# Performance work log

Hardware: AMD Instinct MI355X
Metric: run time of the kernel (lower is better)

Reference implementation:

```python
import jax, jax.numpy as jnp
import numpy as np

BLOCKSIZE = 128
NUM_EXPERTS = 16
TOP_K = 6
HIDDEN = 2048
INTER = 1408
TOKENS = 4096
N_BLK_H = HIDDEN // BLOCKSIZE   # 16
N_BLK_I = -(-INTER // BLOCKSIZE)  # 11 (ceil)


def setup_inputs() -> dict:
    key = jax.random.key(0)
    ks = jax.random.split(key, 8)
    x = jax.random.normal(ks[0], (TOKENS, HIDDEN), dtype=jnp.float32)
    selected_experts = jax.random.randint(ks[1], (TOKENS, TOP_K), 0, NUM_EXPERTS)
    # quantized-style weights + per-block scales (dequant = w * repeat(s, blocksize))
    w0 = jax.random.normal(ks[2], (NUM_EXPERTS, INTER, HIDDEN), dtype=jnp.float32) * 0.02
    s0 = jax.random.uniform(ks[3], (NUM_EXPERTS, INTER, N_BLK_H), dtype=jnp.float32, minval=0.5, maxval=1.5)
    w1 = jax.random.normal(ks[4], (NUM_EXPERTS, INTER, HIDDEN), dtype=jnp.float32) * 0.02
    s1 = jax.random.uniform(ks[5], (NUM_EXPERTS, INTER, N_BLK_H), dtype=jnp.float32, minval=0.5, maxval=1.5)
    w2 = jax.random.normal(ks[6], (NUM_EXPERTS, HIDDEN, INTER), dtype=jnp.float32) * 0.02
    s2 = jax.random.uniform(ks[7], (NUM_EXPERTS, HIDDEN, N_BLK_I), dtype=jnp.float32, minval=0.5, maxval=1.5)
    return {"x": x, "selected_experts": selected_experts,
            "w0": w0, "s0": s0, "w1": w1, "s1": s1, "w2": w2, "s2": s2}


def _dequant(w, s):
    # w: [E, O, I], s: [E, O, ceil(I/bs)] -> broadcast each scale over its block
    s_full = jnp.repeat(s, BLOCKSIZE, axis=-1)[..., : w.shape[-1]]
    return w * s_full


def reference(x, selected_experts, w0, s0, w1, s1, w2, s2):
    # Dequantize block-quantized expert weights.
    W0 = _dequant(w0, s0)  # gate proj [E, I, H]
    W1 = _dequant(w1, s1)  # up proj   [E, I, H]
    W2 = _dequant(w2, s2)  # down proj [E, H, I]
    # Original loops token x slot, calling expert(x[i]). Equivalent batched form:
    # compute every expert on every token, then gather by (token, slot) index.
    gate = jnp.einsum('th,eih->eti', x, W0)            # [E, T, I]
    up = jnp.einsum('th,eih->eti', x, W1)              # [E, T, I]
    act = jax.nn.silu(gate) * up                       # [E, T, I]
    all_out = jnp.einsum('eti,ehi->eth', act, W2)      # [E, T, H]
    tok = jnp.arange(x.shape[0])[:, None]              # [T, 1]
    out = all_out[selected_experts, tok]               # [T, K, H]
    return out
```

## Files before the change

### kernel.cpp

```cpp
#include <hip/hip_runtime.h>
#include <stdint.h>

#define TOKENS 4096
#define HIDDEN 2048
#define INTER  1408
#define NEXP   16
#define TOPK   6
#define NPAIR  (TOKENS*TOPK)
#define BM     128
#define MAXTILES (NPAIR/BM + NEXP)
#define MAXT2  (NPAIR/256 + NEXP)
#define NT1    (INTER/128)
#define NT2    (HIDDEN/128)

typedef __attribute__((ext_vector_type(8))) short bf16x8;
typedef __attribute__((ext_vector_type(4))) float f32x4;

__device__ __forceinline__ short f2bf(float f){
  union { float f; uint32_t u; } v; v.f = f;
  uint32_t r = (v.u + 0x7FFFu + ((v.u >> 16) & 1u)) >> 16;
  return (short)(r & 0xFFFFu);
}

__device__ __forceinline__ void gld16(const void* g, const void* l){
  __builtin_amdgcn_global_load_lds((const __attribute__((address_space(1))) void*)g,
                                   (__attribute__((address_space(3))) void*)l, 16, 0, 0);
}


__global__ void k_xcast(const float* __restrict__ x, short* __restrict__ xb){
  int i = (blockIdx.x * 256 + threadIdx.x) * 8;
  f32x4 a = *(const f32x4*)(x + i);
  f32x4 b = *(const f32x4*)(x + i + 4);
  bf16x8 o;
  #pragma unroll
  for (int j = 0; j < 4; ++j){ o[j] = f2bf(a[j]); o[4+j] = f2bf(b[j]); }
  *(bf16x8*)(xb + i) = o;
}

__global__ void k_dequant(const float* __restrict__ w, const float* __restrict__ s,
                          short* __restrict__ o, int rowlen, int nblk){
  const int row = blockIdx.x;
  const size_t base = (size_t)row * rowlen;
  for (int c = threadIdx.x * 8; c < rowlen; c += blockDim.x * 8){
    float sc = s[(size_t)row * nblk + (c >> 7)];
    f32x4 a = *(const f32x4*)(w + base + c);
    f32x4 b = *(const f32x4*)(w + base + c + 4);
    bf16x8 h;
    #pragma unroll
    for (int j = 0; j < 4; ++j){ h[j] = f2bf(a[j] * sc); h[4+j] = f2bf(b[j] * sc); }
    *(bf16x8*)(o + base + c) = h;
  }
}

__global__ void k_count(const int* __restrict__ sel, int* __restrict__ cnt){
  int p = blockIdx.x * 256 + threadIdx.x;
  if (p < NPAIR) atomicAdd(&cnt[sel[p]], 1);
}

__global__ void k_scan(const int* __restrict__ cnt, int* __restrict__ offsets,
                       int2* __restrict__ tiles, int* __restrict__ ntiles,
                       int2* __restrict__ tiles2, int* __restrict__ ntiles2){
  if (threadIdx.x != 0) return;
  int off = 0, nt = 0, nt2 = 0;
  for (int e = 0; e < NEXP; ++e){
    offsets[e] = off;
    int c = cnt[e];
    for (int m = 0; m < c; m += BM){
      int rows = c - m; if (rows > BM) rows = BM;
      tiles[nt++] = make_int2(off + m, (e << 16) | rows);
    }
    for (int m = 0; m < c; m += 256){
      int rows = c - m; if (rows > 256) rows = 256;
      tiles2[nt2++] = make_int2(off + m, (e << 16) | rows);
    }
    off += c;
  }
  offsets[NEXP] = off;
  *ntiles = nt;
  *ntiles2 = nt2;
}

__global__ void k_scatter(const int* __restrict__ sel, const int* __restrict__ offsets,
                          int* __restrict__ cursor, int* __restrict__ pair_tk){
  int p = blockIdx.x * 256 + threadIdx.x;
  if (p >= NPAIR) return;
  int e = sel[p];
  int pos = offsets[e] + atomicAdd(&cursor[e], 1);
  pair_tk[pos] = (p / TOPK) * 8 + (p % TOPK);
}


__global__ __launch_bounds__(512) void k_g1(
    const short* __restrict__ xb,
    const short* __restrict__ w0b, const short* __restrict__ w1b,
    const int2* __restrict__ tiles2, const int* __restrict__ ntiles2,
    const int* __restrict__ pair_tk, short* __restrict__ act)
{
  const int nwg = MAXT2 * NT1;
  const int orig = (int)(blockIdx.y * MAXT2 + blockIdx.x);
  const int wg = (orig & 7) * (nwg >> 3) + (orig >> 3);
  const int tx = wg % MAXT2, ty = wg / MAXT2;
  if (tx >= *ntiles2) return;
  const int2 td = tiles2[tx];
  const int mstart = td.x;
  const int e  = td.y >> 16;
  const int vr = td.y & 0xFFFF;

  __shared__ short lA[2][256 * 64];
  __shared__ short lB[2][256 * 64];

  const int tid = threadIdx.x, w = tid >> 6, lane = tid & 63;

  const short* pA[4]; const short* pB[4]; int s8[4];
  #pragma unroll
  for (int i = 0; i < 4; ++i){
    int s = w * 256 + i * 64 + lane;
    int r = s >> 3, g = (s & 7) ^ (r & 7);
    s8[i] = s * 8;
    int p = mstart + r; if (p >= NPAIR) p = NPAIR - 1;
    pA[i] = xb + (size_t)(pair_tk[p] >> 3) * HIDDEN + g * 8;
    int G = r >> 4, srow = (G >> 1) * 16 + (r & 15);
    const short* wsrc = (G & 1) ? w1b : w0b;
    pB[i] = wsrc + ((size_t)e * INTER + (size_t)ty * 128 + srow) * HIDDEN + g * 8;
  }
  auto stage = [&](short* bA, short* bB, int ko){
    #pragma unroll
    for (int i = 0; i < 4; ++i) gld16(pA[i] + ko, bA + s8[i]);
    #pragma unroll
    for (int i = 0; i < 4; ++i) gld16(pB[i] + ko, bB + s8[i]);
  };

  f32x4 acc[4][8];
  #pragma unroll
  for (int i = 0; i < 4; ++i)
    #pragma unroll
    for (int j = 0; j < 8; ++j) acc[i][j] = (f32x4)0.f;

  const int cc = lane & 15, ks = lane >> 4;
  const int sx0 = (ks ^ (cc & 7)) * 8;
  const int sx1 = ((4 | ks) ^ (cc & 7)) * 8;
  const int wm = w >> 1, wn = w & 1;
  int arow[4], brow[8];
  #pragma unroll
  for (int mf = 0; mf < 4; ++mf) arow[mf] = (wm * 64 + mf * 16 + cc) * 64;
  #pragma unroll
  for (int nf = 0; nf < 8; ++nf) brow[nf] = (wn * 128 + nf * 16 + cc) * 64;

  stage(lA[0], lB[0], 0);
  stage(lA[1], lB[1], 64);

  #pragma unroll 1
  for (int kt = 0; kt < 32; ++kt){
    const short* A = lA[kt & 1];
    const short* B = lB[kt & 1];
    if (kt < 31) asm volatile("s_waitcnt vmcnt(8)" ::: "memory");
    else         asm volatile("s_waitcnt vmcnt(0)" ::: "memory");
    __builtin_amdgcn_sched_barrier(0);
    __builtin_amdgcn_s_barrier();
    __builtin_amdgcn_sched_barrier(0);

    bf16x8 a0[4], a1[4];
    #pragma unroll
    for (int mf = 0; mf < 4; ++mf){
      a0[mf] = *(const bf16x8*)(A + arow[mf] + sx0);
      a1[mf] = *(const bf16x8*)(A + arow[mf] + sx1);
    }
    #pragma unroll
    for (int h = 0; h < 2; ++h){
      bf16x8 b0[4], b1[4];
      #pragma unroll
      for (int q = 0; q < 4; ++q){
        b0[q] = *(const bf16x8*)(B + brow[h * 4 + q] + sx0);
        b1[q] = *(const bf16x8*)(B + brow[h * 4 + q] + sx1);
      }
      #pragma unroll
      for (int q = 0; q < 4; ++q)
        #pragma unroll
        for (int mf = 0; mf < 4; ++mf)
          acc[mf][h*4+q] = __builtin_amdgcn_mfma_f32_16x16x32_bf16(a0[mf], b0[q], acc[mf][h*4+q], 0, 0, 0);
      #pragma unroll
      for (int q = 0; q < 4; ++q)
        #pragma unroll
        for (int mf = 0; mf < 4; ++mf)
          acc[mf][h*4+q] = __builtin_amdgcn_mfma_f32_16x16x32_bf16(a1[mf], b1[q], acc[mf][h*4+q], 0, 0, 0);
    }
    __builtin_amdgcn_sched_barrier(0);
    __builtin_amdgcn_s_barrier();
    __builtin_amdgcn_sched_barrier(0);
    if (kt + 2 < 32) stage(lA[kt & 1], lB[kt & 1], (kt + 2) * 64);
  }

  #pragma unroll
  for (int mf = 0; mf < 4; ++mf){
    #pragma unroll
    for (int j = 0; j < 4; ++j){
      int row = wm * 64 + mf * 16 + ks * 4 + j;
      if (row < vr){
        short* ar = act + (size_t)(mstart + row) * INTER + (size_t)ty * 128 + cc;
        #pragma unroll
        for (int q = 0; q < 4; ++q){
          float g = acc[mf][2*q][j], u = acc[mf][2*q+1][j];
          float a = g / (1.f + __expf(-g)) * u;
          ar[(wn * 4 + q) * 16] = f2bf(a);
        }
      }
    }
  }
}

__global__ __launch_bounds__(512) void k_g2(
    const short* __restrict__ act, const short* __restrict__ w2b,
    const int2* __restrict__ tiles2, const int* __restrict__ ntiles2,
    const int* __restrict__ pair_tk, float* __restrict__ out)
{
  const int nwg = MAXT2 * NT2;
  const int orig = (int)(blockIdx.y * MAXT2 + blockIdx.x);
  const int wg = (orig & 7) * (nwg >> 3) + (orig >> 3);
  const int tx = wg % MAXT2, ty = wg / MAXT2;
  if (tx >= *ntiles2) return;
  const int2 td = tiles2[tx];
  const int mstart = td.x;
  const int e  = td.y >> 16;
  const int vr = td.y & 0xFFFF;

  __shared__ short lA[2][256 * 64];
  __shared__ short lB[2][128 * 64];

  const int tid = threadIdx.x, w = tid >> 6, lane = tid & 63;

  const short* pA[4]; int s8a[4];
  #pragma unroll
  for (int i = 0; i < 4; ++i){
    int s = w * 256 + i * 64 + lane;
    int r = s >> 3, g = (s & 7) ^ (r & 7);
    s8a[i] = s * 8;
    int p = mstart + r; if (p >= NPAIR) p = NPAIR - 1;
    pA[i] = act + (size_t)p * INTER + g * 8;
  }
  const short* pB[2]; int s8b[2];
  #pragma unroll
  for (int i = 0; i < 2; ++i){
    int s = w * 128 + i * 64 + lane;
    int r = s >> 3, g = (s & 7) ^ (r & 7);
    s8b[i] = s * 8;
    pB[i] = w2b + ((size_t)e * HIDDEN + (size_t)ty * 128 + r) * INTER + g * 8;
  }
  auto stage = [&](short* bA, short* bB, int ko){
    #pragma unroll
    for (int i = 0; i < 4; ++i) gld16(pA[i] + ko, bA + s8a[i]);
    #pragma unroll
    for (int i = 0; i < 2; ++i) gld16(pB[i] + ko, bB + s8b[i]);
  };

  f32x4 acc[4][4];
  #pragma unroll
  for (int i = 0; i < 4; ++i)
    #pragma unroll
    for (int j = 0; j < 4; ++j) acc[i][j] = (f32x4)0.f;

  const int cc = lane & 15, ks = lane >> 4;
  const int sx0 = (ks ^ (cc & 7)) * 8;
  const int sx1 = ((4 | ks) ^ (cc & 7)) * 8;
  const int wm = w >> 1, wn = w & 1;
  int arow[4], brow[4];
  #pragma unroll
  for (int mf = 0; mf < 4; ++mf) arow[mf] = (wm * 64 + mf * 16 + cc) * 64;
  #pragma unroll
  for (int nf = 0; nf < 4; ++nf) brow[nf] = (wn * 64 + nf * 16 + cc) * 64;

  stage(lA[0], lB[0], 0);
  stage(lA[1], lB[1], 64);

  #pragma unroll 1
  for (int kt = 0; kt < 22; ++kt){
    const short* A = lA[kt & 1];
    const short* B = lB[kt & 1];
    if (kt < 21) asm volatile("s_waitcnt vmcnt(6)" ::: "memory");
    else         asm volatile("s_waitcnt vmcnt(0)" ::: "memory");
    __builtin_amdgcn_sched_barrier(0);
    __builtin_amdgcn_s_barrier();
    __builtin_amdgcn_sched_barrier(0);

    bf16x8 a0[4], a1[4], b0[4], b1[4];
    #pragma unroll
    for (int mf = 0; mf < 4; ++mf){
      a0[mf] = *(const bf16x8*)(A + arow[mf] + sx0);
      a1[mf] = *(const bf16x8*)(A + arow[mf] + sx1);
    }
    #pragma unroll
    for (int nf = 0; nf < 4; ++nf){
      b0[nf] = *(const bf16x8*)(B + brow[nf] + sx0);
      b1[nf] = *(const bf16x8*)(B + brow[nf] + sx1);
    }
    #pragma unroll
    for (int nf = 0; nf < 4; ++nf)
      #pragma unroll
      for (int mf = 0; mf < 4; ++mf)
        acc[mf][nf] = __builtin_amdgcn_mfma_f32_16x16x32_bf16(a0[mf], b0[nf], acc[mf][nf], 0, 0, 0);
    #pragma unroll
    for (int nf = 0; nf < 4; ++nf)
      #pragma unroll
      for (int mf = 0; mf < 4; ++mf)
        acc[mf][nf] = __builtin_amdgcn_mfma_f32_16x16x32_bf16(a1[mf], b1[nf], acc[mf][nf], 0, 0, 0);

    __builtin_amdgcn_sched_barrier(0);
    __builtin_amdgcn_s_barrier();
    __builtin_amdgcn_sched_barrier(0);
    if (kt + 2 < 22) stage(lA[kt & 1], lB[kt & 1], (kt + 2) * 64);
  }

  #pragma unroll
  for (int mf = 0; mf < 4; ++mf){
    #pragma unroll
    for (int j = 0; j < 4; ++j){
      int row = wm * 64 + mf * 16 + ks * 4 + j;
      if (row < vr){
        int ptk = pair_tk[mstart + row];
        float* orow = out + ((size_t)(ptk >> 3) * TOPK + (ptk & 7)) * HIDDEN
                      + (size_t)ty * 128 + wn * 64 + cc;
        #pragma unroll
        for (int nf = 0; nf < 4; ++nf)
          orow[nf * 16] = acc[mf][nf][j];
      }
    }
  }
}


__global__ __launch_bounds__(256) void k_gemm1(
    const short* __restrict__ xb,
    const float* __restrict__ w0, const float* __restrict__ s0,
    const float* __restrict__ w1, const float* __restrict__ s1,
    const int2* __restrict__ tiles, const int* __restrict__ ntiles,
    const int* __restrict__ pair_tk, short* __restrict__ act)
{
  if ((int)blockIdx.x >= *ntiles) return;
  const int2 td = tiles[blockIdx.x];
  const int mstart = td.x;
  const int e  = td.y >> 16;
  const int vr = td.y & 0xFFFF;
  const int tid = threadIdx.x;
  const int lane = tid & 63;

  __shared__ short lA[BM * 32];
  __shared__ short lB0[BM * 40];
  __shared__ short lB1[BM * 40];

  const int r0 = tid >> 2, r1 = 64 + (tid >> 2);
  const int seg = tid & 3;
  int p0 = mstart + r0; if (p0 >= NPAIR) p0 = NPAIR - 1;
  int p1 = mstart + r1; if (p1 >= NPAIR) p1 = NPAIR - 1;
  const short* arow0 = xb + (size_t)(pair_tk[p0] >> 3) * HIDDEN + (seg ^ ((r0 >> 1) & 3)) * 8;
  const short* arow1 = xb + (size_t)(pair_tk[p1] >> 3) * HIDDEN + (seg ^ ((r1 >> 1) & 3)) * 8;
  const short* ldsA0 = &lA[tid * 8];
  const short* ldsA1 = &lA[2048 + tid * 8];

  const int brow = tid >> 1, half = tid & 1;
  const int gbrow = blockIdx.y * BM + brow;
  const float* w0row = w0 + ((size_t)e * INTER + gbrow) * HIDDEN + half * 16;
  const float* w1row = w1 + ((size_t)e * INTER + gbrow) * HIDDEN + half * 16;
  const float* s0row = s0 + ((size_t)e * INTER + gbrow) * (HIDDEN / 128);
  const float* s1row = s1 + ((size_t)e * INTER + gbrow) * (HIDDEN / 128);
  short* lb0w = &lB0[brow * 40 + half * 16];
  short* lb1w = &lB1[brow * 40 + half * 16];

  f32x4 acc0[4][4], acc1[4][4];
  #pragma unroll
  for (int i = 0; i < 4; ++i)
    #pragma unroll
    for (int j = 0; j < 4; ++j){ acc0[i][j] = (f32x4)0.f; acc1[i][j] = (f32x4)0.f; }

  const int wm = tid >> 7, wn = (tid >> 6) & 1;
  const int cc = lane & 15, ks = lane >> 4;

  for (int kt = 0; kt < HIDDEN / 32; ++kt){
    gld16(arow0 + kt * 32, ldsA0);
    gld16(arow1 + kt * 32, ldsA1);
    {
      float sc = s0row[kt >> 2];
      const float* g = w0row + kt * 32;
      f32x4 q0 = *(const f32x4*)g,       q1 = *(const f32x4*)(g + 4),
            q2 = *(const f32x4*)(g + 8), q3 = *(const f32x4*)(g + 12);
      bf16x8 h0, h1;
      #pragma unroll
      for (int i = 0; i < 4; ++i){
        h0[i] = f2bf(q0[i] * sc); h0[4 + i] = f2bf(q1[i] * sc);
        h1[i] = f2bf(q2[i] * sc); h1[4 + i] = f2bf(q3[i] * sc);
      }
      *(bf16x8*)lb0w = h0; *(bf16x8*)(lb0w + 8) = h1;
    }
    {
      float sc = s1row[kt >> 2];
      const float* g = w1row + kt * 32;
      f32x4 q0 = *(const f32x4*)g,       q1 = *(const f32x4*)(g + 4),
            q2 = *(const f32x4*)(g + 8), q3 = *(const f32x4*)(g + 12);
      bf16x8 h0, h1;
      #pragma unroll
      for (int i = 0; i < 4; ++i){
        h0[i] = f2bf(q0[i] * sc); h0[4 + i] = f2bf(q1[i] * sc);
        h1[i] = f2bf(q2[i] * sc); h1[4 + i] = f2bf(q3[i] * sc);
      }
      *(bf16x8*)lb1w = h0; *(bf16x8*)(lb1w + 8) = h1;
    }
    __syncthreads();

    bf16x8 af[4];
    #pragma unroll
    for (int mf = 0; mf < 4; ++mf){
      int row = wm * 64 + mf * 16 + cc;
      af[mf] = *(const bf16x8*)&lA[row * 32 + ((ks ^ ((row >> 1) & 3)) * 8)];
    }
    #pragma unroll
    for (int nf = 0; nf < 4; ++nf){
      int rb = wn * 64 + nf * 16 + cc;
      bf16x8 b0 = *(const bf16x8*)&lB0[rb * 40 + ks * 8];
      bf16x8 b1 = *(const bf16x8*)&lB1[rb * 40 + ks * 8];
      #pragma unroll
      for (int mf = 0; mf < 4; ++mf)
        acc0[mf][nf] = __builtin_amdgcn_mfma_f32_16x16x32_bf16(af[mf], b0, acc0[mf][nf], 0, 0, 0);
      #pragma unroll
      for (int mf = 0; mf < 4; ++mf)
        acc1[mf][nf] = __builtin_amdgcn_mfma_f32_16x16x32_bf16(af[mf], b1, acc1[mf][nf], 0, 0, 0);
    }
    __syncthreads();
  }

  const int rbase = wm * 64 + (lane >> 4) * 4;
  #pragma unroll
  for (int mf = 0; mf < 4; ++mf){
    #pragma unroll
    for (int j = 0; j < 4; ++j){
      int row = rbase + mf * 16 + j;
      if (row < vr){
        short* ar = act + (size_t)(mstart + row) * INTER + blockIdx.y * BM + wn * 64 + cc;
        #pragma unroll
        for (int nf = 0; nf < 4; ++nf){
          float g = acc0[mf][nf][j], u = acc1[mf][nf][j];
          float a = g / (1.f + __expf(-g)) * u;
          ar[nf * 16] = f2bf(a);
        }
      }
    }
  }
}

__global__ __launch_bounds__(256) void k_gemm2(
    const short* __restrict__ act,
    const float* __restrict__ w2, const float* __restrict__ s2,
    const int2* __restrict__ tiles, const int* __restrict__ ntiles,
    const int* __restrict__ pair_tk, float* __restrict__ out)
{
  if ((int)blockIdx.x >= *ntiles) return;
  const int2 td = tiles[blockIdx.x];
  const int mstart = td.x;
  const int e  = td.y >> 16;
  const int vr = td.y & 0xFFFF;
  const int tid = threadIdx.x;
  const int lane = tid & 63;

  __shared__ short lA[BM * 32];
  __shared__ short lB[BM * 40];

  const int r0 = tid >> 2, r1 = 64 + (tid >> 2);
  const int seg = tid & 3;
  int p0 = mstart + r0; if (p0 >= NPAIR) p0 = NPAIR - 1;
  int p1 = mstart + r1; if (p1 >= NPAIR) p1 = NPAIR - 1;
  const short* arow0 = act + (size_t)p0 * INTER + (seg ^ ((r0 >> 1) & 3)) * 8;
  const short* arow1 = act + (size_t)p1 * INTER + (seg ^ ((r1 >> 1) & 3)) * 8;
  const short* ldsA0 = &lA[tid * 8];
  const short* ldsA1 = &lA[2048 + tid * 8];

  const int brow = tid >> 1, half = tid & 1;
  const int gbrow = blockIdx.y * BM + brow;
  const float* w2row = w2 + ((size_t)e * HIDDEN + gbrow) * INTER + half * 16;
  const float* s2row = s2 + ((size_t)e * HIDDEN + gbrow) * 11;
  short* lbw = &lB[brow * 40 + half * 16];

  f32x4 acc[4][4];
  #pragma unroll
  for (int i = 0; i < 4; ++i)
    #pragma unroll
    for (int j = 0; j < 4; ++j) acc[i][j] = (f32x4)0.f;

  const int wm = tid >> 7, wn = (tid >> 6) & 1;
  const int cc = lane & 15, ks = lane >> 4;

  for (int kt = 0; kt < INTER / 32; ++kt){
    gld16(arow0 + kt * 32, ldsA0);
    gld16(arow1 + kt * 32, ldsA1);
    {
      float sc = s2row[kt >> 2];
      const float* g = w2row + kt * 32;
      f32x4 q0 = *(const f32x4*)g,       q1 = *(const f32x4*)(g + 4),
            q2 = *(const f32x4*)(g + 8), q3 = *(const f32x4*)(g + 12);
      bf16x8 h0, h1;
      #pragma unroll
      for (int i = 0; i < 4; ++i){
        h0[i] = f2bf(q0[i] * sc); h0[4 + i] = f2bf(q1[i] * sc);
        h1[i] = f2bf(q2[i] * sc); h1[4 + i] = f2bf(q3[i] * sc);
      }
      *(bf16x8*)lbw = h0; *(bf16x8*)(lbw + 8) = h1;
    }
    __syncthreads();

    bf16x8 af[4];
    #pragma unroll
    for (int mf = 0; mf < 4; ++mf){
      int row = wm * 64 + mf * 16 + cc;
      af[mf] = *(const bf16x8*)&lA[row * 32 + ((ks ^ ((row >> 1) & 3)) * 8)];
    }
    #pragma unroll
    for (int nf = 0; nf < 4; ++nf){
      int rb = wn * 64 + nf * 16 + cc;
      bf16x8 b = *(const bf16x8*)&lB[rb * 40 + ks * 8];
      #pragma unroll
      for (int mf = 0; mf < 4; ++mf)
        acc[mf][nf] = __builtin_amdgcn_mfma_f32_16x16x32_bf16(af[mf], b, acc[mf][nf], 0, 0, 0);
    }
    __syncthreads();
  }

  const int rbase = wm * 64 + (lane >> 4) * 4;
  #pragma unroll
  for (int mf = 0; mf < 4; ++mf){
    #pragma unroll
    for (int j = 0; j < 4; ++j){
      int row = rbase + mf * 16 + j;
      if (row < vr){
        int ptk = pair_tk[mstart + row];
        float* orow = out + ((size_t)(ptk >> 3) * TOPK + (ptk & 7)) * HIDDEN
                      + blockIdx.y * BM + wn * 64 + cc;
        #pragma unroll
        for (int nf = 0; nf < 4; ++nf)
          orow[nf * 16] = acc[mf][nf][j];
      }
    }
  }
}


extern "C" void kernel_launch(void* const* d_in, const int* in_sizes, int n_in,
                              void* d_out, int out_size, void* d_ws, size_t ws_size,
                              hipStream_t stream)
{
  const float* x  = (const float*)d_in[0];
  const int*   sel= (const int*)  d_in[1];
  const float* w0 = (const float*)d_in[2];
  const float* s0 = (const float*)d_in[3];
  const float* w1 = (const float*)d_in[4];
  const float* s1 = (const float*)d_in[5];
  const float* w2 = (const float*)d_in[6];
  const float* s2 = (const float*)d_in[7];
  float* out = (float*)d_out;

  char* ws = (char*)d_ws;
  size_t o = 0;
  auto alloc = [&](size_t n){ size_t r = o; o = (o + n + 255) & ~(size_t)255; return r; };
  int*  cnt     = (int*) (ws + alloc(64));
  int*  cursor  = (int*) (ws + alloc(64));
  int*  offsets = (int*) (ws + alloc(68));
  int*  ntiles  = (int*) (ws + alloc(4));
  int*  ntiles2 = (int*) (ws + alloc(4));
  int2* tiles   = (int2*)(ws + alloc(MAXTILES * 8));
  int2* tiles2  = (int2*)(ws + alloc(MAXT2 * 8));
  int*  pair_tk = (int*) (ws + alloc((size_t)NPAIR * 4));
  short* xb     = (short*)(ws + alloc((size_t)TOKENS * HIDDEN * 2));
  short* act    = (short*)(ws + alloc((size_t)NPAIR * INTER * 2));
  const size_t WSZ = (size_t)NEXP * INTER * HIDDEN * 2;
  short* w0b    = (short*)(ws + alloc(WSZ));
  short* w1b    = (short*)(ws + alloc(WSZ));
  short* w2b    = (short*)(ws + alloc(WSZ));
  const bool predeq = (ws_size >= o);
  (void)in_sizes; (void)n_in; (void)out_size;

  hipMemsetAsync(ws, 0, 512, stream);

  k_xcast  <<<(TOKENS * HIDDEN) / (256 * 8), 256, 0, stream>>>(x, xb);
  k_count  <<<(NPAIR + 255) / 256, 256, 0, stream>>>(sel, cnt);
  k_scan   <<<1, 64, 0, stream>>>(cnt, offsets, tiles, ntiles, tiles2, ntiles2);
  k_scatter<<<(NPAIR + 255) / 256, 256, 0, stream>>>(sel, offsets, cursor, pair_tk);

  if (predeq){
    k_dequant<<<NEXP * INTER,  256, 0, stream>>>(w0, s0, w0b, HIDDEN, HIDDEN / 128);
    k_dequant<<<NEXP * INTER,  256, 0, stream>>>(w1, s1, w1b, HIDDEN, HIDDEN / 128);
    k_dequant<<<NEXP * HIDDEN, 256, 0, stream>>>(w2, s2, w2b, INTER, 11);
    k_g1<<<dim3(MAXT2, NT1), 512, 0, stream>>>(xb, w0b, w1b,
                                               tiles2, ntiles2, pair_tk, act);
    k_g2<<<dim3(MAXT2, NT2), 512, 0, stream>>>(act, w2b,
                                               tiles2, ntiles2, pair_tk, out);
  } else {
    k_gemm1<<<dim3(MAXTILES, NT1), 256, 0, stream>>>(xb, w0, s0, w1, s1,
                                                     tiles, ntiles, pair_tk, act);
    k_gemm2<<<dim3(MAXTILES, NT2), 256, 0, stream>>>(act, w2, s2,
                                                     tiles, ntiles, pair_tk, out);
  }
}
```

Measured before the change: 984.3 us.

## Interleave LDS reads with MFMA in sub-phases using barriers and setprio

Both grouped GEMM kernels now split each k-step into smaller sub-phases. Each sub-phase loads only the B fragments it needs from LDS, waits at a barrier, and then issues MFMAs at raised wave priority via s_setprio. This keeps waves in lockstep so the LDS reads of one wave overlap the matrix work of another, in a ping-pong style. It also moves the global prefetch and its vmcnt wait to the end of the iteration, so the wait covers the next buffer. The cost is several extra workgroup barriers per k-step, which may add synchronisation overhead.

```diff
diff --git a/kernel.cpp b/kernel.cpp
--- a/kernel.cpp
+++ b/kernel.cpp
@@ -149,46 +149,62 @@
 
   stage(lA[0], lB[0], 0);
   stage(lA[1], lB[1], 64);
+  asm volatile("s_waitcnt vmcnt(8)" ::: "memory");
+  __builtin_amdgcn_sched_barrier(0);
+  __builtin_amdgcn_s_barrier();
+  __builtin_amdgcn_sched_barrier(0);
 
   #pragma unroll 1
   for (int kt = 0; kt < 32; ++kt){
     const short* A = lA[kt & 1];
     const short* B = lB[kt & 1];
-    if (kt < 31) asm volatile("s_waitcnt vmcnt(8)" ::: "memory");
-    else         asm volatile("s_waitcnt vmcnt(0)" ::: "memory");
+    bf16x8 a0[4], a1[4];
+
+    #pragma unroll
+    for (int q = 0; q < 4; ++q){
+      if (q == 0){
+        #pragma unroll
+        for (int mf = 0; mf < 4; ++mf){
+          a0[mf] = *(const bf16x8*)(A + arow[mf] + sx0);
+          a1[mf] = *(const bf16x8*)(A + arow[mf] + sx1);
+        }
+      }
+      bf16x8 b0[2], b1[2];
+      #pragma unroll
+      for (int j = 0; j < 2; ++j){
+        b0[j] = *(const bf16x8*)(B + brow[2*q+j] + sx0);
+        b1[j] = *(const bf16x8*)(B + brow[2*q+j] + sx1);
+      }
+      __builtin_amdgcn_sched_barrier(0);
+      __builtin_amdgcn_s_barrier();
+      asm volatile("s_waitcnt lgkmcnt(0)" ::: "memory");
+      __builtin_amdgcn_sched_barrier(0);
+      __builtin_amdgcn_s_setprio(1);
+      #pragma unroll
+      for (int j = 0; j < 2; ++j)
+        #pragma unroll
+        for (int mf = 0; mf < 4; ++mf)
+          acc[mf][2*q+j] = __builtin_amdgcn_mfma_f32_16x16x32_bf16(a0[mf], b0[j], acc[mf][2*q+j], 0, 0, 0);
+      #pragma unroll
+      for (int j = 0; j < 2; ++j)
+        #pragma unroll
+        for (int mf = 0; mf < 4; ++mf)
+          acc[mf][2*q+j] = __builtin_amdgcn_mfma_f32_16x16x32_bf16(a1[mf], b1[j], acc[mf][2*q+j], 0, 0, 0);
+      __builtin_amdgcn_s_setprio(0);
+      __builtin_amdgcn_sched_barrier(0);
+      __builtin_amdgcn_s_barrier();
+      __builtin_amdgcn_sched_barrier(0);
+    }
+
+    if (kt + 2 < 32){
+      stage(lA[kt & 1], lB[kt & 1], (kt + 2) * 64);
+      asm volatile("s_waitcnt vmcnt(8)" ::: "memory");
+    } else {
+      asm volatile("s_waitcnt vmcnt(0)" ::: "memory");
+    }
     __builtin_amdgcn_sched_barrier(0);
     __builtin_amdgcn_s_barrier();
     __builtin_amdgcn_sched_barrier(0);
-
-    bf16x8 a0[4], a1[4];
-    #pragma unroll
-    for (int mf = 0; mf < 4; ++mf){
-      a0[mf] = *(const bf16x8*)(A + arow[mf] + sx0);
-      a1[mf] = *(const bf16x8*)(A + arow[mf] + sx1);
-    }
-    #pragma unroll
-    for (int h = 0; h < 2; ++h){
-      bf16x8 b0[4], b1[4];
-      #pragma unroll
-      for (int q = 0; q < 4; ++q){
-        b0[q] = *(const bf16x8*)(B + brow[h * 4 + q] + sx0);
-        b1[q] = *(const bf16x8*)(B + brow[h * 4 + q] + sx1);
-      }
-      #pragma unroll
-      for (int q = 0; q < 4; ++q)
-        #pragma unroll
-        for (int mf = 0; mf < 4; ++mf)
-          acc[mf][h*4+q] = __builtin_amdgcn_mfma_f32_16x16x32_bf16(a0[mf], b0[q], acc[mf][h*4+q], 0, 0, 0);
-      #pragma unroll
-      for (int q = 0; q < 4; ++q)
-        #pragma unroll
-        for (int mf = 0; mf < 4; ++mf)
-          acc[mf][h*4+q] = __builtin_amdgcn_mfma_f32_16x16x32_bf16(a1[mf], b1[q], acc[mf][h*4+q], 0, 0, 0);
-    }
-    __builtin_amdgcn_sched_barrier(0);
-    __builtin_amdgcn_s_barrier();
-    __builtin_amdgcn_sched_barrier(0);
-    if (kt + 2 < 32) stage(lA[kt & 1], lB[kt & 1], (kt + 2) * 64);
   }
 
   #pragma unroll
@@ -271,43 +287,62 @@
 
   stage(lA[0], lB[0], 0);
   stage(lA[1], lB[1], 64);
+  asm volatile("s_waitcnt vmcnt(6)" ::: "memory");
+  __builtin_amdgcn_sched_barrier(0);
+  __builtin_amdgcn_s_barrier();
+  __builtin_amdgcn_sched_barrier(0);
 
   #pragma unroll 1
   for (int kt = 0; kt < 22; ++kt){
     const short* A = lA[kt & 1];
     const short* B = lB[kt & 1];
-    if (kt < 21) asm volatile("s_waitcnt vmcnt(6)" ::: "memory");
-    else         asm volatile("s_waitcnt vmcnt(0)" ::: "memory");
+    bf16x8 a0[4], a1[4];
+
+    #pragma unroll
+    for (int q = 0; q < 2; ++q){
+      if (q == 0){
+        #pragma unroll
+        for (int mf = 0; mf < 4; ++mf){
+          a0[mf] = *(const bf16x8*)(A + arow[mf] + sx0);
+          a1[mf] = *(const bf16x8*)(A + arow[mf] + sx1);
+        }
+      }
+      bf16x8 b0[2], b1[2];
+      #pragma unroll
+      for (int j = 0; j < 2; ++j){
+        b0[j] = *(const bf16x8*)(B + brow[2*q+j] + sx0);
+        b1[j] = *(const bf16x8*)(B + brow[2*q+j] + sx1);
+      }
+      __builtin_amdgcn_sched_barrier(0);
+      __builtin_amdgcn_s_barrier();
+      asm volatile("s_waitcnt lgkmcnt(0)" ::: "memory");
+      __builtin_amdgcn_sched_barrier(0);
+      __builtin_amdgcn_s_setprio(1);
+      #pragma unroll
+      for (int j = 0; j < 2; ++j)
+        #pragma unroll
+        for (int mf = 0; mf < 4; ++mf)
+          acc[mf][2*q+j] = __builtin_amdgcn_mfma_f32_16x16x32_bf16(a0[mf], b0[j], acc[mf][2*q+j], 0, 0, 0);
+      #pragma unroll
+      for (int j = 0; j < 2; ++j)
+        #pragma unroll
+        for (int mf = 0; mf < 4; ++mf)
+          acc[mf][2*q+j] = __builtin_amdgcn_mfma_f32_16x16x32_bf16(a1[mf], b1[j], acc[mf][2*q+j], 0, 0, 0);
+      __builtin_amdgcn_s_setprio(0);
+      __builtin_amdgcn_sched_barrier(0);
+      __builtin_amdgcn_s_barrier();
+      __builtin_amdgcn_sched_barrier(0);
+    }
+
+    if (kt + 2 < 22){
+      stage(lA[kt & 1], lB[kt & 1], (kt + 2) * 64);
+      asm volatile("s_waitcnt vmcnt(6)" ::: "memory");
+    } else {
+      asm volatile("s_waitcnt vmcnt(0)" ::: "memory");
+    }
     __builtin_amdgcn_sched_barrier(0);
     __builtin_amdgcn_s_barrier();
     __builtin_amdgcn_sched_barrier(0);
-
-    bf16x8 a0[4], a1[4], b0[4], b1[4];
-    #pragma unroll
-    for (int mf = 0; mf < 4; ++mf){
-      a0[mf] = *(const bf16x8*)(A + arow[mf] + sx0);
-      a1[mf] = *(const bf16x8*)(A + arow[mf] + sx1);
-    }
-    #pragma unroll
-    for (int nf = 0; nf < 4; ++nf){
-      b0[nf] = *(const bf16x8*)(B + brow[nf] + sx0);
-      b1[nf] = *(const bf16x8*)(B + brow[nf] + sx1);
-    }
-    #pragma unroll
-    for (int nf = 0; nf < 4; ++nf)
-      #pragma unroll
-      for (int mf = 0; mf < 4; ++mf)
-        acc[mf][nf] = __builtin_amdgcn_mfma_f32_16x16x32_bf16(a0[mf], b0[nf], acc[mf][nf], 0, 0, 0);
-    #pragma unroll
-    for (int nf = 0; nf < 4; ++nf)
-      #pragma unroll
-      for (int mf = 0; mf < 4; ++mf)
-        acc[mf][nf] = __builtin_amdgcn_mfma_f32_16x16x32_bf16(a1[mf], b1[nf], acc[mf][nf], 0, 0, 0);
-
-    __builtin_amdgcn_sched_barrier(0);
-    __builtin_amdgcn_s_barrier();
-    __builtin_amdgcn_sched_barrier(0);
-    if (kt + 2 < 22) stage(lA[kt & 1], lB[kt & 1], (kt + 2) * 64);
   }
 
   #pragma unroll
```

Result: slower. 1.070 ms (+8.7%).

## Split K-tiles into four 32-wide LDS stages with interleaved prefetch in MoE GEMMs

Applied to the files above, without the earlier changes.

Both grouped GEMM kernels now use four LDS buffers of 32-wide K slices instead of two 64-wide ones. Each half-step issues the next global-to-LDS prefetch between its LDS reads and its MFMA block, and raises wave priority around the MFMAs. The XOR swizzle is dropped for a plain 4-chunk row layout, which may add LDS bank conflicts. The w2 dequant launch is also moved after the first GEMM; same-stream ordering is kept, so that move alone changes little.

```diff
diff --git a/kernel.cpp b/kernel.cpp
--- a/kernel.cpp
+++ b/kernel.cpp
@@ -26,6 +26,11 @@
   __builtin_amdgcn_global_load_lds((const __attribute__((address_space(1))) void*)g,
                                    (__attribute__((address_space(3))) void*)l, 16, 0, 0);
 }
+
+#define SB() __builtin_amdgcn_sched_barrier(0)
+#define BAR() __builtin_amdgcn_s_barrier()
+#define WAITV(n) asm volatile("s_waitcnt vmcnt(" #n ")" ::: "memory")
+#define WAITL() asm volatile("s_waitcnt lgkmcnt(0)" ::: "memory")
 
 
 __global__ void k_xcast(const float* __restrict__ x, short* __restrict__ xb){
@@ -107,28 +112,28 @@
   const int e  = td.y >> 16;
   const int vr = td.y & 0xFFFF;
 
-  __shared__ short lA[2][256 * 64];
-  __shared__ short lB[2][256 * 64];
+  __shared__ short lA[4][8192];
+  __shared__ short lB[4][8192];
 
   const int tid = threadIdx.x, w = tid >> 6, lane = tid & 63;
 
-  const short* pA[4]; const short* pB[4]; int s8[4];
-  #pragma unroll
-  for (int i = 0; i < 4; ++i){
-    int s = w * 256 + i * 64 + lane;
-    int r = s >> 3, g = (s & 7) ^ (r & 7);
-    s8[i] = s * 8;
+  const short* pA[2]; const short* pB[2]; int sg8[2];
+  #pragma unroll
+  for (int i = 0; i < 2; ++i){
+    int s = (w * 2 + i) * 64 + lane;
+    int r = s >> 2, j = s & 3;
+    sg8[i] = s * 8;
     int p = mstart + r; if (p >= NPAIR) p = NPAIR - 1;
-    pA[i] = xb + (size_t)(pair_tk[p] >> 3) * HIDDEN + g * 8;
+    pA[i] = xb + (size_t)(pair_tk[p] >> 3) * HIDDEN + j * 8;
     int G = r >> 4, srow = (G >> 1) * 16 + (r & 15);
     const short* wsrc = (G & 1) ? w1b : w0b;
-    pB[i] = wsrc + ((size_t)e * INTER + (size_t)ty * 128 + srow) * HIDDEN + g * 8;
-  }
-  auto stage = [&](short* bA, short* bB, int ko){
-    #pragma unroll
-    for (int i = 0; i < 4; ++i) gld16(pA[i] + ko, bA + s8[i]);
-    #pragma unroll
-    for (int i = 0; i < 4; ++i) gld16(pB[i] + ko, bB + s8[i]);
+    pB[i] = wsrc + ((size_t)e * INTER + (size_t)ty * 128 + srow) * HIDDEN + j * 8;
+  }
+  auto stage = [&](int slot, int ko){
+    #pragma unroll
+    for (int i = 0; i < 2; ++i) gld16(pA[i] + ko, &lA[slot][sg8[i]]);
+    #pragma unroll
+    for (int i = 0; i < 2; ++i) gld16(pB[i] + ko, &lB[slot][sg8[i]]);
   };
 
   f32x4 acc[4][8];
@@ -138,57 +143,59 @@
     for (int j = 0; j < 8; ++j) acc[i][j] = (f32x4)0.f;
 
   const int cc = lane & 15, ks = lane >> 4;
-  const int sx0 = (ks ^ (cc & 7)) * 8;
-  const int sx1 = ((4 | ks) ^ (cc & 7)) * 8;
+  const int kso = ks * 8;
   const int wm = w >> 1, wn = w & 1;
   int arow[4], brow[8];
   #pragma unroll
-  for (int mf = 0; mf < 4; ++mf) arow[mf] = (wm * 64 + mf * 16 + cc) * 64;
-  #pragma unroll
-  for (int nf = 0; nf < 8; ++nf) brow[nf] = (wn * 128 + nf * 16 + cc) * 64;
-
-  stage(lA[0], lB[0], 0);
-  stage(lA[1], lB[1], 64);
+  for (int mf = 0; mf < 4; ++mf) arow[mf] = (wm * 64 + mf * 16 + cc) * 32;
+  #pragma unroll
+  for (int nf = 0; nf < 8; ++nf) brow[nf] = (wn * 128 + nf * 16 + cc) * 32;
+
+  stage(0, 0); stage(1, 32); stage(2, 64); stage(3, 96);
 
   #pragma unroll 1
-  for (int kt = 0; kt < 32; ++kt){
-    const short* A = lA[kt & 1];
-    const short* B = lB[kt & 1];
-    if (kt < 31) asm volatile("s_waitcnt vmcnt(8)" ::: "memory");
-    else         asm volatile("s_waitcnt vmcnt(0)" ::: "memory");
-    __builtin_amdgcn_sched_barrier(0);
-    __builtin_amdgcn_s_barrier();
-    __builtin_amdgcn_sched_barrier(0);
-
-    bf16x8 a0[4], a1[4];
-    #pragma unroll
-    for (int mf = 0; mf < 4; ++mf){
-      a0[mf] = *(const bf16x8*)(A + arow[mf] + sx0);
-      a1[mf] = *(const bf16x8*)(A + arow[mf] + sx1);
-    }
-    #pragma unroll
-    for (int h = 0; h < 2; ++h){
-      bf16x8 b0[4], b1[4];
-      #pragma unroll
-      for (int q = 0; q < 4; ++q){
-        b0[q] = *(const bf16x8*)(B + brow[h * 4 + q] + sx0);
-        b1[q] = *(const bf16x8*)(B + brow[h * 4 + q] + sx1);
-      }
-      #pragma unroll
-      for (int q = 0; q < 4; ++q)
+  for (int t = 0; t < 32; ++t){
+    const int b = t & 1;
+    if (t == 0)      { WAITV(12); }
+    else if (t < 31) { WAITV(8);  }
+    else             { WAITV(4);  }
+    SB(); BAR(); SB();
+    {
+      bf16x8 a0[4], bb[8];
+      #pragma unroll
+      for (int mf = 0; mf < 4; ++mf) a0[mf] = *(const bf16x8*)&lA[b*2][arow[mf] + kso];
+      #pragma unroll
+      for (int nf = 0; nf < 8; ++nf) bb[nf] = *(const bf16x8*)&lB[b*2][brow[nf] + kso];
+      if (t >= 1 && t + 1 < 32) stage(((t+1)&1)*2 + 1, (t+1)*64 + 32);
+      WAITL(); SB();
+      __builtin_amdgcn_s_setprio(1);
+      #pragma unroll
+      for (int nf = 0; nf < 8; ++nf)
         #pragma unroll
         for (int mf = 0; mf < 4; ++mf)
-          acc[mf][h*4+q] = __builtin_amdgcn_mfma_f32_16x16x32_bf16(a0[mf], b0[q], acc[mf][h*4+q], 0, 0, 0);
-      #pragma unroll
-      for (int q = 0; q < 4; ++q)
+          acc[mf][nf] = __builtin_amdgcn_mfma_f32_16x16x32_bf16(a0[mf], bb[nf], acc[mf][nf], 0, 0, 0);
+      __builtin_amdgcn_s_setprio(0);
+      SB(); BAR(); SB();
+    }
+    if (t < 31) { WAITV(8); } else { WAITV(0); }
+    SB(); BAR(); SB();
+    {
+      bf16x8 a0[4], bb[8];
+      #pragma unroll
+      for (int mf = 0; mf < 4; ++mf) a0[mf] = *(const bf16x8*)&lA[b*2+1][arow[mf] + kso];
+      #pragma unroll
+      for (int nf = 0; nf < 8; ++nf) bb[nf] = *(const bf16x8*)&lB[b*2+1][brow[nf] + kso];
+      if (t + 2 < 32) stage(b*2, (t+2)*64);
+      WAITL(); SB();
+      __builtin_amdgcn_s_setprio(1);
+      #pragma unroll
+      for (int nf = 0; nf < 8; ++nf)
         #pragma unroll
         for (int mf = 0; mf < 4; ++mf)
-          acc[mf][h*4+q] = __builtin_amdgcn_mfma_f32_16x16x32_bf16(a1[mf], b1[q], acc[mf][h*4+q], 0, 0, 0);
-    }
-    __builtin_amdgcn_sched_barrier(0);
-    __builtin_amdgcn_s_barrier();
-    __builtin_amdgcn_sched_barrier(0);
-    if (kt + 2 < 32) stage(lA[kt & 1], lB[kt & 1], (kt + 2) * 64);
+          acc[mf][nf] = __builtin_amdgcn_mfma_f32_16x16x32_bf16(a0[mf], bb[nf], acc[mf][nf], 0, 0, 0);
+      __builtin_amdgcn_s_setprio(0);
+      SB(); BAR(); SB();
+    }
   }
 
   #pragma unroll
@@ -224,33 +231,31 @@
   const int e  = td.y >> 16;
   const int vr = td.y & 0xFFFF;
 
-  __shared__ short lA[2][256 * 64];
-  __shared__ short lB[2][128 * 64];
+  __shared__ short lA[4][8192];
+  __shared__ short lB[4][4096];
 
   const int tid = threadIdx.x, w = tid >> 6, lane = tid & 63;
 
-  const short* pA[4]; int s8a[4];
-  #pragma unroll
-  for (int i = 0; i < 4; ++i){
-    int s = w * 256 + i * 64 + lane;
-    int r = s >> 3, g = (s & 7) ^ (r & 7);
-    s8a[i] = s * 8;
+  const short* pA[2]; int sg8[2];
+  #pragma unroll
+  for (int i = 0; i < 2; ++i){
+    int s = (w * 2 + i) * 64 + lane;
+    int r = s >> 2, j = s & 3;
+    sg8[i] = s * 8;
     int p = mstart + r; if (p >= NPAIR) p = NPAIR - 1;
-    pA[i] = act + (size_t)p * INTER + g * 8;
-  }
-  const short* pB[2]; int s8b[2];
-  #pragma unroll
-  for (int i = 0; i < 2; ++i){
-    int s = w * 128 + i * 64 + lane;
-    int r = s >> 3, g = (s & 7) ^ (r & 7);
-    s8b[i] = s * 8;
-    pB[i] = w2b + ((size_t)e * HIDDEN + (size_t)ty * 128 + r) * INTER + g * 8;
-  }
-  auto stage = [&](short* bA, short* bB, int ko){
-    #pragma unroll
-    for (int i = 0; i < 4; ++i) gld16(pA[i] + ko, bA + s8a[i]);
-    #pragma unroll
-    for (int i = 0; i < 2; ++i) gld16(pB[i] + ko, bB + s8b[i]);
+    pA[i] = act + (size_t)p * INTER + j * 8;
+  }
+  const short* pB; int sb8;
+  {
+    int s = tid;
+    int r = s >> 2, j = s & 3;
+    sb8 = s * 8;
+    pB = w2b + ((size_t)e * HIDDEN + (size_t)ty * 128 + r) * INTER + j * 8;
+  }
+  auto stage = [&](int slot, int ko){
+    #pragma unroll
+    for (int i = 0; i < 2; ++i) gld16(pA[i] + ko, &lA[slot][sg8[i]]);
+    gld16(pB + ko, &lB[slot][sb8]);
   };
 
   f32x4 acc[4][4];
@@ -260,54 +265,59 @@
     for (int j = 0; j < 4; ++j) acc[i][j] = (f32x4)0.f;
 
   const int cc = lane & 15, ks = lane >> 4;
-  const int sx0 = (ks ^ (cc & 7)) * 8;
-  const int sx1 = ((4 | ks) ^ (cc & 7)) * 8;
+  const int kso = ks * 8;
   const int wm = w >> 1, wn = w & 1;
   int arow[4], brow[4];
   #pragma unroll
-  for (int mf = 0; mf < 4; ++mf) arow[mf] = (wm * 64 + mf * 16 + cc) * 64;
-  #pragma unroll
-  for (int nf = 0; nf < 4; ++nf) brow[nf] = (wn * 64 + nf * 16 + cc) * 64;
-
-  stage(lA[0], lB[0], 0);
-  stage(lA[1], lB[1], 64);
+  for (int mf = 0; mf < 4; ++mf) arow[mf] = (wm * 64 + mf * 16 + cc) * 32;
+  #pragma unroll
+  for (int nf = 0; nf < 4; ++nf) brow[nf] = (wn * 64 + nf * 16 + cc) * 32;
+
+  stage(0, 0); stage(1, 32); stage(2, 64); stage(3, 96);
 
   #pragma unroll 1
-  for (int kt = 0; kt < 22; ++kt){
-    const short* A = lA[kt & 1];
-    const short* B = lB[kt & 1];
-    if (kt < 21) asm volatile("s_waitcnt vmcnt(6)" ::: "memory");
-    else         asm volatile("s_waitcnt vmcnt(0)" ::: "memory");
-    __builtin_amdgcn_sched_barrier(0);
-    __builtin_amdgcn_s_barrier();
-    __builtin_amdgcn_sched_barrier(0);
-
-    bf16x8 a0[4], a1[4], b0[4], b1[4];
-    #pragma unroll
-    for (int mf = 0; mf < 4; ++mf){
-      a0[mf] = *(const bf16x8*)(A + arow[mf] + sx0);
-      a1[mf] = *(const bf16x8*)(A + arow[mf] + sx1);
-    }
-    #pragma unroll
-    for (int nf = 0; nf < 4; ++nf){
-      b0[nf] = *(const bf16x8*)(B + brow[nf] + sx0);
-      b1[nf] = *(const bf16x8*)(B + brow[nf] + sx1);
-    }
-    #pragma unroll
-    for (int nf = 0; nf < 4; ++nf)
-      #pragma unroll
-      for (int mf = 0; mf < 4; ++mf)
-        acc[mf][nf] = __builtin_amdgcn_mfma_f32_16x16x32_bf16(a0[mf], b0[nf], acc[mf][nf], 0, 0, 0);
-    #pragma unroll
-    for (int nf = 0; nf < 4; ++nf)
-      #pragma unroll
-      for (int mf = 0; mf < 4; ++mf)
-        acc[mf][nf] = __builtin_amdgcn_mfma_f32_16x16x32_bf16(a1[mf], b1[nf], acc[mf][nf], 0, 0, 0);
-
-    __builtin_amdgcn_sched_barrier(0);
-    __builtin_amdgcn_s_barrier();
-    __builtin_amdgcn_sched_barrier(0);
-    if (kt + 2 < 22) stage(lA[kt & 1], lB[kt & 1], (kt + 2) * 64);
+  for (int t = 0; t < 22; ++t){
+    const int b = t & 1;
+    if (t == 0)      { WAITV(9); }
+    else if (t < 21) { WAITV(6); }
+    else             { WAITV(3); }
+    SB(); BAR(); SB();
+    {
+      bf16x8 a0[4], bb[4];
+      #pragma unroll
+      for (int mf = 0; mf < 4; ++mf) a0[mf] = *(const bf16x8*)&lA[b*2][arow[mf] + kso];
+      #pragma unroll
+      for (int nf = 0; nf < 4; ++nf) bb[nf] = *(const bf16x8*)&lB[b*2][brow[nf] + kso];
+      if (t >= 1 && t + 1 < 22) stage(((t+1)&1)*2 + 1, (t+1)*64 + 32);
+      WAITL(); SB();
+      __builtin_amdgcn_s_setprio(1);
+      #pragma unroll
+      for (int nf = 0; nf < 4; ++nf)
+        #pragma unroll
+        for (int mf = 0; mf < 4; ++mf)
+          acc[mf][nf] = __builtin_amdgcn_mfma_f32_16x16x32_bf16(a0[mf], bb[nf], acc[mf][nf], 0, 0, 0);
+      __builtin_amdgcn_s_setprio(0);
+      SB(); BAR(); SB();
+    }
+    if (t < 21) { WAITV(6); } else { WAITV(0); }
+    SB(); BAR(); SB();
+    {
+      bf16x8 a0[4], bb[4];
+      #pragma unroll
+      for (int mf = 0; mf < 4; ++mf) a0[mf] = *(const bf16x8*)&lA[b*2+1][arow[mf] + kso];
+      #pragma unroll
+      for (int nf = 0; nf < 4; ++nf) bb[nf] = *(const bf16x8*)&lB[b*2+1][brow[nf] + kso];
+      if (t + 2 < 22) stage(b*2, (t+2)*64);
+      WAITL(); SB();
+      __builtin_amdgcn_s_setprio(1);
+      #pragma unroll
+      for (int nf = 0; nf < 4; ++nf)
+        #pragma unroll
+        for (int mf = 0; mf < 4; ++mf)
+          acc[mf][nf] = __builtin_amdgcn_mfma_f32_16x16x32_bf16(a0[mf], bb[nf], acc[mf][nf], 0, 0, 0);
+      __builtin_amdgcn_s_setprio(0);
+      SB(); BAR(); SB();
+    }
   }
 
   #pragma unroll
@@ -584,9 +594,9 @@
   if (predeq){
     k_dequant<<<NEXP * INTER,  256, 0, stream>>>(w0, s0, w0b, HIDDEN, HIDDEN / 128);
     k_dequant<<<NEXP * INTER,  256, 0, stream>>>(w1, s1, w1b, HIDDEN, HIDDEN / 128);
-    k_dequant<<<NEXP * HIDDEN, 256, 0, stream>>>(w2, s2, w2b, INTER, 11);
     k_g1<<<dim3(MAXT2, NT1), 512, 0, stream>>>(xb, w0b, w1b,
                                                tiles2, ntiles2, pair_tk, act);
+    k_dequant<<<NEXP * HIDDEN, 256, 0, stream>>>(w2, s2, w2b, INTER, 11);
     k_g2<<<dim3(MAXT2, NT2), 512, 0, stream>>>(act, w2b,
                                                tiles2, ntiles2, pair_tk, out);
   } else {
```

Measured after the change: 937.0 us. 4.8% less time.
